# Optimization experiments

Measured on AMD Instinct MI355X. Metric: run time of the kernel, lower is better.

The kernel has to match this reference:

```python
import jax, jax.numpy as jnp
import numpy as np

D_MODEL = 1024
NUM_HEADS = 16


def setup_inputs() -> dict:
    key = jax.random.key(0)
    ks = jax.random.split(key, 6)
    B, N, L, C = 16, 1024, 120, D_MODEL
    s = 0.02
    return {
        "x": jax.random.normal(ks[0], (B, N, C), jnp.float32),
        "cond": jax.random.normal(ks[1], (B, L, C), jnp.float32),
        "mask": jax.random.randint(ks[2], (B, L), 0, 2, jnp.int32),
        "Wq": jax.random.normal(ks[3], (C, C), jnp.float32) * s,
        "bq": jnp.zeros((C,), jnp.float32),
        "Wkv": jax.random.normal(ks[4], (2 * C, C), jnp.float32) * s,
        "bkv": jnp.zeros((2 * C,), jnp.float32),
        "Wp": jax.random.normal(ks[5], (C, C), jnp.float32) * s,
        "bp": jnp.zeros((C,), jnp.float32),
    }


def reference(x, cond, mask, Wq, bq, Wkv, bkv, Wp, bp):
    B, N, C = x.shape
    H = NUM_HEADS
    Dh = C // H
    scale = Dh ** (-0.5)
    # q: (B,H,N,Dh)
    q = (x @ Wq.T + bq).reshape(B, N, H, Dh).transpose(0, 2, 1, 3)
    # kv: (2,B,H,L,Dh)
    L = cond.shape[1]
    kv = (cond @ Wkv.T + bkv).reshape(B, L, 2, H, Dh).transpose(2, 0, 3, 1, 4)
    k, v = kv[0], kv[1]
    # attention scores (B,H,N,L)
    attn = jnp.einsum("bhnd,bhld->bhnl", q, k) * scale
    attn = jnp.where(mask[:, None, None, :] == 0, -jnp.inf, attn)
    attn = jax.nn.softmax(attn, axis=-1)
    out = jnp.einsum("bhnl,bhld->bhnd", attn, v)  # (B,H,N,Dh)
    out = out.transpose(0, 2, 1, 3).reshape(B, N, C)
    return out @ Wp.T + bp
```

## Files before the change

### kernel.cpp

```cpp
#include <hip/hip_runtime.h>

typedef unsigned short u16;
typedef unsigned int u32;
typedef float f32x4 __attribute__((ext_vector_type(4)));
typedef __bf16 bf16x8 __attribute__((ext_vector_type(8)));
typedef u32 u32x4 __attribute__((ext_vector_type(4)));
typedef u16 u16x4 __attribute__((ext_vector_type(4)));

#define NB 16
#define NSEQ 1024
#define NL 120
#define NLP 128
#define NC 1024
#define NH 16
#define NDH 64
#define KSP 72
#define VTP 136

__device__ __forceinline__ u16 f2bf(float f) {
  u32 u = __float_as_uint(f);
  return (u16)((u + 0x7fffu + ((u >> 16) & 1u)) >> 16);
}

__device__ __forceinline__ void gld_lds16(const void* g, void* l) {
  __builtin_amdgcn_global_load_lds(
      (const __attribute__((address_space(1))) void*)g,
      (__attribute__((address_space(3))) void*)l, 16, 0, 0);
}

#define SBAR()                               \
  do {                                       \
    __builtin_amdgcn_sched_barrier(0);       \
    __builtin_amdgcn_s_barrier();            \
    __builtin_amdgcn_sched_barrier(0);       \
  } while (0)
#define VMW(n)                                          \
  do {                                                  \
    __builtin_amdgcn_sched_barrier(0);                  \
    asm volatile("s_waitcnt vmcnt(" #n ")" ::: "memory"); \
  } while (0)
#define SB0() __builtin_amdgcn_sched_barrier(0)

__global__ __launch_bounds__(256) void cast_all(
    const float* __restrict__ x, u16* __restrict__ xb,
    const float* __restrict__ cond, u16* __restrict__ condb,
    const float* __restrict__ Wq, u16* __restrict__ Wqb,
    const float* __restrict__ Wkv, u16* __restrict__ Wkvb,
    const float* __restrict__ Wp, u16* __restrict__ Wpb) {
  int bk = blockIdx.x;
  const float* src;
  u16* dst;
  if (bk < 16384) { src = x; dst = xb; }
  else if (bk < 18304) { src = cond; dst = condb; bk -= 16384; }
  else if (bk < 19328) { src = Wq; dst = Wqb; bk -= 18304; }
  else if (bk < 21376) { src = Wkv; dst = Wkvb; bk -= 19328; }
  else { src = Wp; dst = Wpb; bk -= 21376; }
  size_t i = ((size_t)bk * 256 + threadIdx.x) * 4;
  f32x4 v = *(const f32x4*)(src + i);
  u16x4 o;
  o.x = f2bf(v.x); o.y = f2bf(v.y); o.z = f2bf(v.z); o.w = f2bf(v.w);
  *(u16x4*)(dst + i) = o;
}

template <bool OUT_F32>
__global__ __launch_bounds__(256) void gemm_bt(
    const u16* __restrict__ A, const u16* __restrict__ Bt,
    const float* __restrict__ bias, void* __restrict__ Cout,
    int M, int Nn, int K) {
  __shared__ u16 As[128 * 32];
  __shared__ u16 Bs[128 * 32];
  const int mt = M >> 7;
  const int bm = (int)blockIdx.x % mt;
  const int bn = (int)blockIdx.x / mt;
  const int m0 = bm << 7, n0 = bn << 7;
  const int tid = threadIdx.x;
  const int w = tid >> 6, lane = tid & 63;
  const int wm = (w & 1) << 6, wn = (w >> 1) << 6;
  const int quad = lane >> 4, l15 = lane & 15;

  f32x4 acc[4][4];
#pragma unroll
  for (int i = 0; i < 4; ++i)
#pragma unroll
    for (int j = 0; j < 4; ++j) acc[i][j] = (f32x4){0.f, 0.f, 0.f, 0.f};

  const int r0 = tid >> 2;
  const int cb = ((((tid & 3) - (r0 >> 1)) & 3)) << 3;
  const u16* aP = A + (size_t)(m0 + r0) * K + cb;
  const u16* bP = Bt + (size_t)(n0 + r0) * K + cb;
  u16* asDst = &As[r0 * 32 + ((tid & 3) << 3)];
  u16* bsDst = &Bs[r0 * 32 + ((tid & 3) << 3)];

  const int sw = ((quad + (l15 >> 1)) & 3) << 3;

  for (int k0 = 0; k0 < K; k0 += 32) {
    __syncthreads();
    gld_lds16(aP + k0, asDst);
    gld_lds16(aP + (size_t)64 * K + k0, asDst + 64 * 32);
    gld_lds16(bP + k0, bsDst);
    gld_lds16(bP + (size_t)64 * K + k0, bsDst + 64 * 32);
    __syncthreads();

    bf16x8 af[4], bfr[4];
#pragma unroll
    for (int i = 0; i < 4; ++i)
      af[i] = *(const bf16x8*)&As[(wm + i * 16 + l15) * 32 + sw];
#pragma unroll
    for (int j = 0; j < 4; ++j)
      bfr[j] = *(const bf16x8*)&Bs[(wn + j * 16 + l15) * 32 + sw];
#pragma unroll
    for (int i = 0; i < 4; ++i)
#pragma unroll
      for (int j = 0; j < 4; ++j)
        acc[i][j] =
            __builtin_amdgcn_mfma_f32_16x16x32_bf16(af[i], bfr[j], acc[i][j], 0, 0, 0);
  }

#pragma unroll
  for (int j = 0; j < 4; ++j) {
    const int col = n0 + wn + j * 16 + l15;
    const float bv = bias[col];
#pragma unroll
    for (int i = 0; i < 4; ++i) {
      const int row = m0 + wm + i * 16 + quad * 4;
#pragma unroll
      for (int r = 0; r < 4; ++r) {
        const float v = acc[i][j][r] + bv;
        if (OUT_F32)
          ((float*)Cout)[(size_t)(row + r) * Nn + col] = v;
        else
          ((u16*)Cout)[(size_t)(row + r) * Nn + col] = f2bf(v);
      }
    }
  }
}

template <bool OUT_F32>
__global__ __launch_bounds__(512, 2) void gemm256(
    const u16* __restrict__ A, const u16* __restrict__ Bt,
    const float* __restrict__ bias, void* __restrict__ Cout,
    int M, int Nn, int K) {
  __shared__ u16 S[2][2][2][8192];

  const int bid = (int)blockIdx.x;
  const int mt = M >> 8;
  const int mpx = mt >> 3;
  const int xcd = bid & 7, idx = bid >> 3;
  const int bm = xcd * mpx + (idx % mpx);
  const int bn = idx / mpx;
  const int m0 = bm << 8, n0 = bn << 8;

  const int tid = threadIdx.x;
  const int w = tid >> 6, lane = tid & 63;
  const int quad = lane >> 4, l15 = lane & 15;
  const int wr = w & 1, wc = w >> 1;

  const int srow = tid >> 3;
  const int xoff = (((tid & 7) ^ (srow & 7)) << 3);
  const u16* aB0 = A + (size_t)(m0 + srow) * K + xoff;
  const u16* bB0 = Bt + (size_t)(n0 + srow) * K + xoff;
  const size_t rowK64 = (size_t)64 * K;
  const size_t rowK128 = (size_t)128 * K;

  auto STAGE = [&](int ab, int buf, int half, int t) {
    const u16* g = (ab ? bB0 : aB0) + half * rowK128 + t * 64;
    u16* d = &S[ab][buf][half][0] + tid * 8;
    gld_lds16(g, d);
    gld_lds16(g + rowK64, d + 4096);
  };

  const int c0 = ((quad << 4) ^ ((l15 & 7) << 4));
  const int c1 = c0 ^ 64;
  const int arow = (wr * 64 + l15) * 128;
  const int brow = (wc * 32 + l15) * 128;

  bf16x8 afA[4][2], afB[4][2], blA[2][2], blB[2][2], bhA[2][2], bhB[2][2];
  auto LDA_TO = [&](bf16x8(&dst)[4][2], int buf, int rh) {
    const char* base = (const char*)&S[0][buf][rh][0] + arow;
#pragma unroll
    for (int f = 0; f < 4; ++f) {
      dst[f][0] = *(const bf16x8*)(base + f * 2048 + c0);
      dst[f][1] = *(const bf16x8*)(base + f * 2048 + c1);
    }
  };
  auto LDB_TO = [&](bf16x8(&dst)[2][2], int buf, int ch) {
    const char* base = (const char*)&S[1][buf][ch][0] + brow;
#pragma unroll
    for (int g = 0; g < 2; ++g) {
      dst[g][0] = *(const bf16x8*)(base + g * 2048 + c0);
      dst[g][1] = *(const bf16x8*)(base + g * 2048 + c1);
    }
  };

  f32x4 a_ll[4][2], a_lh[4][2], a_hh[4][2], a_hl[4][2];
#pragma unroll
  for (int f = 0; f < 4; ++f)
#pragma unroll
    for (int g = 0; g < 2; ++g) {
      a_ll[f][g] = (f32x4){0.f, 0.f, 0.f, 0.f};
      a_lh[f][g] = (f32x4){0.f, 0.f, 0.f, 0.f};
      a_hh[f][g] = (f32x4){0.f, 0.f, 0.f, 0.f};
      a_hl[f][g] = (f32x4){0.f, 0.f, 0.f, 0.f};
    }

  auto MM = [&](f32x4(&acc)[4][2], bf16x8(&af)[4][2], bf16x8(&bf)[2][2]) {
    __builtin_amdgcn_s_setprio(1);
#pragma unroll
    for (int f = 0; f < 4; ++f)
#pragma unroll
      for (int g = 0; g < 2; ++g) {
        acc[f][g] = __builtin_amdgcn_mfma_f32_16x16x32_bf16(af[f][0], bf[g][0],
                                                            acc[f][g], 0, 0, 0);
        acc[f][g] = __builtin_amdgcn_mfma_f32_16x16x32_bf16(af[f][1], bf[g][1],
                                                            acc[f][g], 0, 0, 0);
      }
    __builtin_amdgcn_s_setprio(0);
  };

  const int NT = K >> 6;
  const int NIT = K >> 7;

  STAGE(0, 0, 0, 0); STAGE(0, 0, 1, 0); STAGE(1, 0, 0, 0); STAGE(1, 0, 1, 0);
  STAGE(0, 1, 0, 1); STAGE(1, 1, 1, 1);
  VMW(4);
  SBAR();
  LDA_TO(afA, 0, 0); LDB_TO(blA, 0, 0);
  SB0();

#pragma unroll 1
  for (int it = 0; it < NIT; ++it) {
    const int t1 = 2 * it + 1;
    int t2 = 2 * it + 2; if (t2 > NT - 1) t2 = NT - 1;
    int t3 = 2 * it + 3; if (t3 > NT - 1) t3 = NT - 1;
    STAGE(1, 1, 0, t1);
    SBAR();
    LDB_TO(bhA, 0, 1); SB0();
    MM(a_ll, afA, blA);
    STAGE(0, 1, 1, t1); VMW(6);
    SBAR();
    LDA_TO(afB, 0, 1); SB0();
    MM(a_lh, afA, bhA);
    STAGE(0, 0, 0, t2);
    SBAR();
    MM(a_hh, afB, bhA);
    STAGE(1, 0, 1, t2); VMW(6);
    SBAR();
    LDA_TO(afA, 1, 0); LDB_TO(blB, 1, 0); SB0();
    MM(a_hl, afB, blA);
    STAGE(1, 0, 0, t2);
    SBAR();
    LDB_TO(bhB, 1, 1); SB0();
    MM(a_ll, afA, blB);
    STAGE(0, 0, 1, t2); VMW(6);
    SBAR();
    LDA_TO(afB, 1, 1); SB0();
    MM(a_lh, afA, bhB);
    STAGE(0, 1, 0, t3);
    SBAR();
    MM(a_hh, afB, bhB);
    STAGE(1, 1, 1, t3); VMW(6);
    SBAR();
    LDA_TO(afA, 0, 0); LDB_TO(blA, 0, 0); SB0();
    MM(a_hl, afB, blB);
  }

  auto EPI = [&](f32x4(&acc)[4][2], int rh, int ch) {
#pragma unroll
    for (int g = 0; g < 2; ++g) {
      const int col = n0 + ch * 128 + wc * 32 + g * 16 + l15;
      const float bv = bias[col];
#pragma unroll
      for (int f = 0; f < 4; ++f) {
        const int row = m0 + rh * 128 + wr * 64 + f * 16 + quad * 4;
#pragma unroll
        for (int r = 0; r < 4; ++r) {
          const float v = acc[f][g][r] + bv;
          if (OUT_F32)
            ((float*)Cout)[(size_t)(row + r) * Nn + col] = v;
          else
            ((u16*)Cout)[(size_t)(row + r) * Nn + col] = f2bf(v);
        }
      }
    }
  };
  EPI(a_ll, 0, 0); EPI(a_lh, 0, 1); EPI(a_hh, 1, 1); EPI(a_hl, 1, 0);
}

__global__ __launch_bounds__(256) void attn(
    const u16* __restrict__ Qb, const u16* __restrict__ KVb,
    const int* __restrict__ mask, u16* __restrict__ Ob) {
  __shared__ u16 Ks[NLP * KSP];
  __shared__ u16 Vt[NDH * VTP];
  __shared__ float mb[NLP];
  __shared__ u16 pb[4][16 * VTP];

  const int chunk = (int)blockIdx.x & 3;
  const int h = ((int)blockIdx.x >> 2) & 15;
  const int b = (int)blockIdx.x >> 6;
  const int tid = threadIdx.x;
  const int w = tid >> 6, lane = tid & 63;
  const int quad = lane >> 4, l15 = lane & 15;
  const u16* kvbase = KVb + (size_t)b * NL * 2 * NC;

  for (int i = tid; i < NLP * 8; i += 256) {
    const int l = i >> 3, c8 = (i & 7) * 8;
    u32x4 z = {0u, 0u, 0u, 0u};
    u32x4 v = (l < NL) ? *(const u32x4*)(kvbase + (size_t)l * 2 * NC + h * NDH + c8) : z;
    *(u32x4*)&Ks[l * KSP + c8] = v;
  }
  u16* vstage = &pb[0][0];
  for (int i = tid; i < NL * 8; i += 256) {
    const int l = i >> 3, c8 = (i & 7) * 8;
    *(u32x4*)&vstage[l * NDH + c8] =
        *(const u32x4*)(kvbase + (size_t)l * 2 * NC + NC + h * NDH + c8);
  }
  for (int i = tid; i < NLP; i += 256)
    mb[i] = (i < NL && mask[b * NL + i] != 0) ? 0.0f : -1e30f;
  __syncthreads();
  {
    const int d = tid & 63;
#pragma unroll
    for (int it2 = 0; it2 < 8; ++it2) {
      const int l4 = (tid >> 6) + it2 * 4;
      u16x4 vv;
      if (l4 < 30) {
        vv.x = vstage[(l4 * 4 + 0) * NDH + d];
        vv.y = vstage[(l4 * 4 + 1) * NDH + d];
        vv.z = vstage[(l4 * 4 + 2) * NDH + d];
        vv.w = vstage[(l4 * 4 + 3) * NDH + d];
      } else {
        vv = (u16x4){0, 0, 0, 0};
      }
      *(u16x4*)&Vt[d * VTP + l4 * 4] = vv;
    }
  }
  __syncthreads();

  const float scale = 0.125f;
  const u16* qbase = Qb + (size_t)(b * NSEQ + chunk * 256 + l15) * NC + h * NDH + quad * 8;
  bf16x8 a0 = *(const bf16x8*)(qbase + (size_t)(0 * 64 + w * 16) * NC);
  bf16x8 a1 = *(const bf16x8*)(qbase + (size_t)(0 * 64 + w * 16) * NC + 32);

  for (int it = 0; it < 4; ++it) {
    const int q0 = chunk * 256 + it * 64 + w * 16;
    const int itn = (it + 1) & 3;
    const u16* qn = qbase + (size_t)(itn * 64 + w * 16) * NC;
    const bf16x8 n0 = *(const bf16x8*)qn;
    const bf16x8 n1 = *(const bf16x8*)(qn + 32);

    f32x4 s[8];
#pragma unroll
    for (int kt = 0; kt < 8; ++kt) {
      const u16* kb = &Ks[(kt * 16 + l15) * KSP + quad * 8];
      const bf16x8 b0 = *(const bf16x8*)kb;
      const bf16x8 b1 = *(const bf16x8*)(kb + 32);
      f32x4 t = {0.f, 0.f, 0.f, 0.f};
      t = __builtin_amdgcn_mfma_f32_16x16x32_bf16(a0, b0, t, 0, 0, 0);
      t = __builtin_amdgcn_mfma_f32_16x16x32_bf16(a1, b1, t, 0, 0, 0);
      s[kt] = t;
    }
#pragma unroll
    for (int kt = 0; kt < 8; ++kt) {
      const float mbv = mb[kt * 16 + l15];
#pragma unroll
      for (int r = 0; r < 4; ++r) s[kt][r] = s[kt][r] * scale + mbv;
    }
    float sum[4];
#pragma unroll
    for (int r = 0; r < 4; ++r) {
      float m = s[0][r];
#pragma unroll
      for (int kt = 1; kt < 8; ++kt) m = fmaxf(m, s[kt][r]);
      m = fmaxf(m, __shfl_xor(m, 1));
      m = fmaxf(m, __shfl_xor(m, 2));
      m = fmaxf(m, __shfl_xor(m, 4));
      m = fmaxf(m, __shfl_xor(m, 8));
      float su = 0.f;
#pragma unroll
      for (int kt = 0; kt < 8; ++kt) {
        s[kt][r] = __expf(s[kt][r] - m);
        su += s[kt][r];
      }
      su += __shfl_xor(su, 1);
      su += __shfl_xor(su, 2);
      su += __shfl_xor(su, 4);
      su += __shfl_xor(su, 8);
      sum[r] = su;
    }
#pragma unroll
    for (int r = 0; r < 4; ++r) {
      const float inv = 1.0f / sum[r];
#pragma unroll
      for (int kt = 0; kt < 8; ++kt)
        pb[w][(quad * 4 + r) * VTP + kt * 16 + l15] = f2bf(s[kt][r] * inv);
    }
#pragma unroll
    for (int ntl = 0; ntl < 4; ++ntl) {
      f32x4 o = {0.f, 0.f, 0.f, 0.f};
#pragma unroll
      for (int kt = 0; kt < 4; ++kt) {
        const bf16x8 pa = *(const bf16x8*)&pb[w][l15 * VTP + kt * 32 + quad * 8];
        const bf16x8 vb = *(const bf16x8*)&Vt[(ntl * 16 + l15) * VTP + kt * 32 + quad * 8];
        o = __builtin_amdgcn_mfma_f32_16x16x32_bf16(pa, vb, o, 0, 0, 0);
      }
#pragma unroll
      for (int r = 0; r < 4; ++r)
        Ob[(size_t)(b * NSEQ + q0 + quad * 4 + r) * NC + h * NDH + ntl * 16 + l15] =
            f2bf(o[r]);
    }
    a0 = n0;
    a1 = n1;
  }
}

extern "C" void kernel_launch(void* const* d_in, const int* in_sizes, int n_in,
                              void* d_out, int out_size, void* d_ws, size_t ws_size,
                              hipStream_t stream) {
  const float* x = (const float*)d_in[0];
  const float* cond = (const float*)d_in[1];
  const int* mask = (const int*)d_in[2];
  const float* Wq = (const float*)d_in[3];
  const float* bq = (const float*)d_in[4];
  const float* Wkv = (const float*)d_in[5];
  const float* bkv = (const float*)d_in[6];
  const float* Wp = (const float*)d_in[7];
  const float* bp = (const float*)d_in[8];

  char* ws = (char*)d_ws;
  u16* xb = (u16*)(ws + 0);
  u16* condb = (u16*)(ws + 33554432);
  u16* Wqb = (u16*)(ws + 37486592);
  u16* Wkvb = (u16*)(ws + 39583744);
  u16* Wpb = (u16*)(ws + 43778048);
  u16* Qb = (u16*)(ws + 45875200);
  u16* KVb = (u16*)(ws + 79429632);
  u16* Ob = xb;

  cast_all<<<22400, 256, 0, stream>>>(x, xb, cond, condb, Wq, Wqb, Wkv, Wkvb, Wp, Wpb);

  gemm256<false><<<256, 512, 0, stream>>>(xb, Wqb, bq, Qb, 16384, 1024, 1024);
  gemm_bt<false><<<15 * 16, 256, 0, stream>>>(condb, Wkvb, bkv, KVb, 1920, 2048, 1024);
  attn<<<1024, 256, 0, stream>>>(Qb, KVb, mask, Ob);
  gemm256<true><<<256, 512, 0, stream>>>(Ob, Wpb, bp, d_out, 16384, 1024, 1024);
}
```

Before: 276.9 us.

## Transpose MFMA operands for vectorized epilogue and stage bf16 output through LDS

Swaps the A/B operands of the MFMA so each lane holds four consecutive columns of one row. This lets the fp32 epilogue write 16-byte vector stores and load bias as a float4. For bf16 output, the tile is staged through swizzled LDS and written back as fully coalesced 16-byte rows instead of scattered 2-byte stores. It also moves the afA fragment loads earlier so they overlap the preceding MFMA block. The costs are an extra LDS round trip with two barriers in the bf16 path and reuse of the staging buffer S after the main loop.

After: 275.4 us. No clear change (-0.5%).

```diff
diff --git a/kernel.cpp b/kernel.cpp
--- a/kernel.cpp
+++ b/kernel.cpp
@@ -5,6 +5,7 @@
 typedef float f32x4 __attribute__((ext_vector_type(4)));
 typedef __bf16 bf16x8 __attribute__((ext_vector_type(8)));
 typedef u32 u32x4 __attribute__((ext_vector_type(4)));
+typedef u32 u32x2 __attribute__((ext_vector_type(2)));
 typedef u16 u16x4 __attribute__((ext_vector_type(4)));
 
 #define NB 16
@@ -209,9 +210,9 @@
     for (int f = 0; f < 4; ++f)
 #pragma unroll
       for (int g = 0; g < 2; ++g) {
-        acc[f][g] = __builtin_amdgcn_mfma_f32_16x16x32_bf16(af[f][0], bf[g][0],
+        acc[f][g] = __builtin_amdgcn_mfma_f32_16x16x32_bf16(bf[g][0], af[f][0],
                                                             acc[f][g], 0, 0, 0);
-        acc[f][g] = __builtin_amdgcn_mfma_f32_16x16x32_bf16(af[f][1], bf[g][1],
+        acc[f][g] = __builtin_amdgcn_mfma_f32_16x16x32_bf16(bf[g][1], af[f][1],
                                                             acc[f][g], 0, 0, 0);
       }
     __builtin_amdgcn_s_setprio(0);
@@ -242,10 +243,11 @@
     MM(a_lh, afA, bhA);
     STAGE(0, 0, 0, t2);
     SBAR();
+    LDA_TO(afA, 1, 0); SB0();
     MM(a_hh, afB, bhA);
     STAGE(1, 0, 1, t2); VMW(6);
     SBAR();
-    LDA_TO(afA, 1, 0); LDB_TO(blB, 1, 0); SB0();
+    LDB_TO(blB, 1, 0); SB0();
     MM(a_hl, afB, blA);
     STAGE(1, 0, 0, t2);
     SBAR();
@@ -257,33 +259,69 @@
     MM(a_lh, afA, bhB);
     STAGE(0, 1, 0, t3);
     SBAR();
+    LDA_TO(afA, 0, 0); SB0();
     MM(a_hh, afB, bhB);
     STAGE(1, 1, 1, t3); VMW(6);
     SBAR();
-    LDA_TO(afA, 0, 0); LDB_TO(blA, 0, 0); SB0();
+    LDB_TO(blA, 0, 0); SB0();
     MM(a_hl, afB, blB);
   }
 
-  auto EPI = [&](f32x4(&acc)[4][2], int rh, int ch) {
-#pragma unroll
-    for (int g = 0; g < 2; ++g) {
-      const int col = n0 + ch * 128 + wc * 32 + g * 16 + l15;
-      const float bv = bias[col];
+  f32x4 bv[2][2];
+#pragma unroll
+  for (int ch = 0; ch < 2; ++ch)
+#pragma unroll
+    for (int g = 0; g < 2; ++g)
+      bv[ch][g] = *(const f32x4*)&bias[n0 + ch * 128 + wc * 32 + g * 16 + quad * 4];
+
+  if (OUT_F32) {
+    auto EPI32 = [&](f32x4(&acc)[4][2], int rh, int ch) {
 #pragma unroll
       for (int f = 0; f < 4; ++f) {
-        const int row = m0 + rh * 128 + wr * 64 + f * 16 + quad * 4;
-#pragma unroll
-        for (int r = 0; r < 4; ++r) {
-          const float v = acc[f][g][r] + bv;
-          if (OUT_F32)
-            ((float*)Cout)[(size_t)(row + r) * Nn + col] = v;
-          else
-            ((u16*)Cout)[(size_t)(row + r) * Nn + col] = f2bf(v);
+        const int row = m0 + rh * 128 + wr * 64 + f * 16 + l15;
+#pragma unroll
+        for (int g = 0; g < 2; ++g) {
+          const int col = n0 + ch * 128 + wc * 32 + g * 16 + quad * 4;
+          f32x4 v = acc[f][g] + bv[ch][g];
+          *(f32x4*)&((float*)Cout)[(size_t)row * Nn + col] = v;
         }
       }
-    }
-  };
-  EPI(a_ll, 0, 0); EPI(a_lh, 0, 1); EPI(a_hh, 1, 1); EPI(a_hl, 1, 0);
+    };
+    EPI32(a_ll, 0, 0); EPI32(a_lh, 0, 1); EPI32(a_hh, 1, 1); EPI32(a_hl, 1, 0);
+  } else {
+    asm volatile("s_waitcnt vmcnt(0) lgkmcnt(0)" ::: "memory");
+    __syncthreads();
+    u16* Cs = &S[0][0][0][0];
+    auto STG = [&](f32x4(&acc)[4][2], int rh, int ch) {
+#pragma unroll
+      for (int f = 0; f < 4; ++f) {
+        const int row = rh * 128 + wr * 64 + f * 16 + l15;
+        const int sx = (row & 15) << 2;
+#pragma unroll
+        for (int g = 0; g < 2; ++g) {
+          const int col = ch * 128 + wc * 32 + g * 16 + quad * 4;
+          u16x4 o;
+          o.x = f2bf(acc[f][g][0] + bv[ch][g][0]);
+          o.y = f2bf(acc[f][g][1] + bv[ch][g][1]);
+          o.z = f2bf(acc[f][g][2] + bv[ch][g][2]);
+          o.w = f2bf(acc[f][g][3] + bv[ch][g][3]);
+          *(u16x4*)&Cs[row * 256 + (col ^ sx)] = o;
+        }
+      }
+    };
+    STG(a_ll, 0, 0); STG(a_lh, 0, 1); STG(a_hh, 1, 1); STG(a_hl, 1, 0);
+    __syncthreads();
+#pragma unroll
+    for (int itr = 0; itr < 16; ++itr) {
+      const int row = itr * 16 + w * 2 + (lane >> 5);
+      const int sx = (row & 15) << 2;
+      const int c = (lane & 31) * 8;
+      u32x2 lo = *(const u32x2*)&Cs[row * 256 + (c ^ sx)];
+      u32x2 hi = *(const u32x2*)&Cs[row * 256 + ((c + 4) ^ sx)];
+      u32x4 o = {lo.x, lo.y, hi.x, hi.y};
+      *(u32x4*)&((u16*)Cout)[(size_t)(m0 + row) * Nn + n0 + c] = o;
+    }
+  }
 }
 
 __global__ __launch_bounds__(256) void attn(
```
